# Kernel tuning notes

Hardware: AMD Instinct MI355X
Metric: run time of the kernel (lower is better)

## Reference

```python
import jax, jax.numpy as jnp
import numpy as np

HIDDEN = 128
B, N, S = 4, 200, 512  # batch, 200 segments, 512 tokens each (hard-coded in source view())


def setup_inputs() -> dict:
    key = jax.random.key(0)
    ks = jax.random.split(key, 7)
    query = jax.random.normal(ks[0], (B, HIDDEN), dtype=jnp.float32)
    context = jax.random.normal(ks[1], (B, N, S, HIDDEN), dtype=jnp.float32)
    context_mask = jax.random.uniform(ks[2], (B, N, S), dtype=jnp.float32)
    scale = 1.0 / np.sqrt(HIDDEN)
    Wq = jax.random.normal(ks[3], (HIDDEN, HIDDEN), dtype=jnp.float32) * scale
    bq = jax.random.normal(ks[4], (HIDDEN,), dtype=jnp.float32) * 0.01
    Wc = jax.random.normal(ks[5], (HIDDEN, HIDDEN), dtype=jnp.float32) * scale
    bc = jax.random.normal(ks[6], (HIDDEN,), dtype=jnp.float32) * 0.01
    return {"query": query, "context": context, "context_mask": context_mask,
            "Wq": Wq, "bq": bq, "Wc": Wc, "bc": bc}


def reference(query, context, context_mask, Wq, bq, Wc, bc):
    # q_projection / c_projection (nn.Linear: x @ W.T + b)
    q = query @ Wq.T + bq                      # [B, H]
    c = context @ Wc.T + bc                    # [B, N, S, H]
    # bmm(reshape_c, q) -> scores [B, N, S]
    att = jnp.einsum('bnsh,bh->bns', c, q)
    masked_att = att * context_mask            # multiplicative mask (as in source)
    w = jax.nn.softmax(masked_att, axis=-1)    # [B, N, S]
    # fused dual-axis weighted reductions (avoid [B,N,S,H] broadcast materialization)
    result = jnp.einsum('bns,bnsh->bnh', w, context)       # sum over tokens S
    token_result = jnp.einsum('bns,bnsh->bsh', w, context)  # sum over segments N
    return (result, token_result)
```

## Files before the change

### kernel.cpp

```cpp
#include <hip/hip_runtime.h>
#include <hip/hip_bf16.h>
#include <math.h>

#define H    128
#define NB   4
#define NSEG 200
#define NS   512
#define GN   10
#define GS   64
#define NGRP (NSEG / GN)
#define NST  (NS / GS)

#define RES4 (NB * NSEG * H / 4)
#define TOK4 (NB * NS * H / 4)


__global__ __launch_bounds__(512)
void precompute_kernel(const float* __restrict__ query,
                       const float* __restrict__ Wq,
                       const float* __restrict__ bq,
                       const float* __restrict__ Wc,
                       const float* __restrict__ bc,
                       float* __restrict__ v_out,
                       float* __restrict__ c0_out) {
    __shared__ float WqS[H * (H + 1)];
    __shared__ float qsh[H];
    __shared__ float redv[512];

    const int tid = threadIdx.x;
    const int b   = blockIdx.x;

    for (int i = tid; i < H * H; i += 512)
        WqS[(i >> 7) * (H + 1) + (i & 127)] = Wq[i];
    __syncthreads();

    if (tid < H) {
        float q = bq[tid];
        const float* qr = query + b * H;
        const float* wr = WqS + tid * (H + 1);
        #pragma unroll 8
        for (int k = 0; k < H; ++k) q += qr[k] * wr[k];
        qsh[tid] = q;
    }
    __syncthreads();

    const int h = tid & 127, part = tid >> 7;
    float vp = 0.f;
    #pragma unroll 8
    for (int k = part * 32; k < part * 32 + 32; ++k)
        vp += qsh[k] * Wc[k * H + h];
    redv[tid] = vp;
    __syncthreads();
    if (tid < H)
        v_out[b * H + tid] = redv[tid] + redv[tid + 128] + redv[tid + 256] + redv[tid + 384];

    if (tid < H) redv[tid] = qsh[tid] * bc[tid];
    __syncthreads();
    for (int off = 64; off > 0; off >>= 1) {
        if (tid < off && tid < H / 2) redv[tid] += redv[tid + off];
        __syncthreads();
    }
    if (tid == 0) c0_out[b] = redv[0];
}

__global__ __launch_bounds__(512)
void scores_softmax_kernel(const float* __restrict__ context,
                           const float* __restrict__ mask,
                           const float* __restrict__ v,
                           const float* __restrict__ c0,
                           float* __restrict__ w_out) {
    __shared__ float sc[NS];
    __shared__ float psum[16];
    __shared__ float zinv_sh;

    const int tid = threadIdx.x;
    const int blk = blockIdx.x;
    const int b   = blk / NSEG;
    const float* cseg = context + (size_t)blk * NS * H;
    const float* mrow = mask + (size_t)blk * NS;

    const int   h4  = tid & 31;
    const int   rg  = tid >> 5;
    const float4 vq = ((const float4*)(v + b * H))[h4];
    const float c0b = c0[b];

    float zpart = 0.f;
    #pragma unroll 8
    for (int it = 0; it < NS / 16; ++it) {
        const int s = it * 16 + rg;
        const float4 cv = ((const float4*)(cseg + (size_t)s * H))[h4];
        float p = cv.x * vq.x + cv.y * vq.y + cv.z * vq.z + cv.w * vq.w;
        p += __shfl_xor(p, 16);
        p += __shfl_xor(p, 8);
        p += __shfl_xor(p, 4);
        p += __shfl_xor(p, 2);
        p += __shfl_xor(p, 1);
        if (h4 == 0) {
            const float e = __expf(fminf((p + c0b) * mrow[s], 80.f));
            sc[s] = e;
            zpart += e;
        }
    }
    if (h4 == 0) psum[rg] = zpart;
    __syncthreads();
    if (tid < 64) {
        float t = (tid < 16) ? psum[tid] : 0.f;
        t += __shfl_xor(t, 8);
        t += __shfl_xor(t, 4);
        t += __shfl_xor(t, 2);
        t += __shfl_xor(t, 1);
        if (tid == 0) zinv_sh = 1.f / t;
    }
    __syncthreads();
    w_out[(size_t)blk * NS + tid] = sc[tid] * zinv_sh;
}

__global__ __launch_bounds__(512)
void weighted_kernel(const float* __restrict__ context,
                     const float* __restrict__ w,
                     float* __restrict__ result_part,
                     float* __restrict__ token_part) {
    const int bid = blockIdx.x;
    const int st  = bid & (NST - 1);
    const int tmp = bid / NST;
    const int ng  = tmp % NGRP;
    const int b   = tmp / NGRP;
    const int n0  = ng * GN;
    const int s0  = st * GS;

    const int tid = threadIdx.x;
    const int h4  = tid & 31;
    const int rg  = tid >> 5;

    __shared__ float  wt[GN * GS];
    __shared__ float4 red4[5 * 16 * 32];

    for (int i = tid; i < GN * GS; i += 512) {
        const int nn = i >> 6, ss = i & (GS - 1);
        wt[i] = w[((size_t)(b * NSEG + n0 + nn)) * NS + s0 + ss];
    }
    __syncthreads();

    float4 racc[GN];
    float4 tacc[4];
    #pragma unroll
    for (int n = 0; n < GN; ++n) racc[n] = make_float4(0.f, 0.f, 0.f, 0.f);
    #pragma unroll
    for (int j = 0; j < 4; ++j) tacc[j] = make_float4(0.f, 0.f, 0.f, 0.f);

    #pragma unroll
    for (int n = 0; n < GN; ++n) {
        const float* base = context + ((size_t)(b * NSEG + n0 + n) * NS + s0) * (size_t)H;
        #pragma unroll
        for (int j = 0; j < 4; ++j) {
            const int s = j * 16 + rg;
            const float  wv = wt[n * GS + s];
            const float4 cv = ((const float4*)(base + (size_t)s * H))[h4];
            racc[n].x += wv * cv.x; racc[n].y += wv * cv.y;
            racc[n].z += wv * cv.z; racc[n].w += wv * cv.w;
            tacc[j].x += wv * cv.x; tacc[j].y += wv * cv.y;
            tacc[j].z += wv * cv.z; tacc[j].w += wv * cv.w;
        }
    }

    #pragma unroll
    for (int j = 0; j < 4; ++j) {
        const int s = j * 16 + rg;
        ((float4*)token_part)[(((size_t)ng * NB + b) * NS + s0 + s) * 32 + h4] = tacc[j];
    }

    for (int nb = 0; nb < GN; nb += 5) {
        #pragma unroll
        for (int j = 0; j < 5; ++j)
            red4[(j * 16 + rg) * 32 + h4] = racc[nb + j];
        __syncthreads();
        for (int off = 8; off > 0; off >>= 1) {
            if (rg < off) {
                #pragma unroll
                for (int j = 0; j < 5; ++j) {
                    float4 o = red4[(j * 16 + rg + off) * 32 + h4];
                    float4 mm = red4[(j * 16 + rg) * 32 + h4];
                    mm.x += o.x; mm.y += o.y; mm.z += o.z; mm.w += o.w;
                    red4[(j * 16 + rg) * 32 + h4] = mm;
                }
            }
            __syncthreads();
        }
        if (rg == 0) {
            #pragma unroll
            for (int j = 0; j < 5; ++j)
                ((float4*)result_part)[(((size_t)(b * NSEG + n0 + nb + j)) * NST + st) * 32 + h4]
                    = red4[(j * 16) * 32 + h4];
        }
        __syncthreads();
    }
}

__global__ void combine_kernel(const float* __restrict__ rpart,
                               const float* __restrict__ tpart,
                               float* __restrict__ result_out,
                               float* __restrict__ token_out) {
    const int i = blockIdx.x * blockDim.x + threadIdx.x;
    if (i < RES4) {
        const int row = i >> 5, h4 = i & 31;
        float4 acc = {0.f, 0.f, 0.f, 0.f};
        const float4* p = (const float4*)rpart;
        #pragma unroll
        for (int st = 0; st < NST; ++st) {
            float4 o = p[((size_t)row * NST + st) * 32 + h4];
            acc.x += o.x; acc.y += o.y; acc.z += o.z; acc.w += o.w;
        }
        ((float4*)result_out)[i] = acc;
    } else {
        const int j = i - RES4;
        float4 acc = {0.f, 0.f, 0.f, 0.f};
        const float4* p = (const float4*)tpart;
        #pragma unroll
        for (int g = 0; g < NGRP; ++g) {
            float4 o = p[(size_t)g * TOK4 + j];
            acc.x += o.x; acc.y += o.y; acc.z += o.z; acc.w += o.w;
        }
        ((float4*)token_out)[j] = acc;
    }
}

extern "C" void kernel_launch(void* const* d_in, const int* in_sizes, int n_in,
                              void* d_out, int out_size, void* d_ws, size_t ws_size,
                              hipStream_t stream) {
    const float* query   = (const float*)d_in[0];
    const float* context = (const float*)d_in[1];
    const float* mask    = (const float*)d_in[2];
    const float* Wq      = (const float*)d_in[3];
    const float* bq      = (const float*)d_in[4];
    const float* Wc      = (const float*)d_in[5];
    const float* bc      = (const float*)d_in[6];

    float* out = (float*)d_out;
    float* wsf = (float*)d_ws;

    float* v     = wsf;
    float* c0    = wsf + 512;
    float* w     = wsf + 1024;
    float* rpart = wsf + 1024 + NB * NSEG * NS;
    float* tpart = rpart + NB * NSEG * NST * H;

    float* result_out = out;
    float* token_out  = out + NB * NSEG * H;

    precompute_kernel<<<NB, 512, 0, stream>>>(query, Wq, bq, Wc, bc, v, c0);
    scores_softmax_kernel<<<NB * NSEG, 512, 0, stream>>>(context, mask, v, c0, w);
    weighted_kernel<<<NB * NGRP * NST, 512, 0, stream>>>(context, w, rpart, tpart);
    combine_kernel<<<(RES4 + TOK4) / 256, 256, 0, stream>>>(rpart, tpart, result_out, token_out);
}
```

Measured before the change: 353.7 us.

## Fuse query/context projection precompute into scores kernel and enlarge segment group

Removes the separate precompute launch: each scores/softmax block recomputes q, v = Wc^T q and the bias dot c0 from Wq/Wc, which stay cache-resident. This saves one launch and one dependency bubble, at the cost of redundant projection work in all 800 blocks. The segment group size GN also grows from 10 to 25. That reduces the number of token partial sums written and later combined, but it means fewer weighted-kernel blocks (256 instead of 640) and more accumulator registers per thread.

Result: slower. 411.4 us (+16.3%).

```diff
diff --git a/kernel.cpp b/kernel.cpp
--- a/kernel.cpp
+++ b/kernel.cpp
@@ -6,7 +6,7 @@
 #define NB   4
 #define NSEG 200
 #define NS   512
-#define GN   10
+#define GN   25
 #define GS   64
 #define NGRP (NSEG / GN)
 #define NST  (NS / GS)
@@ -16,59 +16,18 @@
 
 
 __global__ __launch_bounds__(512)
-void precompute_kernel(const float* __restrict__ query,
-                       const float* __restrict__ Wq,
-                       const float* __restrict__ bq,
-                       const float* __restrict__ Wc,
-                       const float* __restrict__ bc,
-                       float* __restrict__ v_out,
-                       float* __restrict__ c0_out) {
-    __shared__ float WqS[H * (H + 1)];
+void scores_softmax_kernel(const float* __restrict__ query,
+                           const float* __restrict__ context,
+                           const float* __restrict__ mask,
+                           const float* __restrict__ Wq,
+                           const float* __restrict__ bq,
+                           const float* __restrict__ Wc,
+                           const float* __restrict__ bc,
+                           float* __restrict__ w_out) {
+    __shared__ float red[512];
     __shared__ float qsh[H];
-    __shared__ float redv[512];
-
-    const int tid = threadIdx.x;
-    const int b   = blockIdx.x;
-
-    for (int i = tid; i < H * H; i += 512)
-        WqS[(i >> 7) * (H + 1) + (i & 127)] = Wq[i];
-    __syncthreads();
-
-    if (tid < H) {
-        float q = bq[tid];
-        const float* qr = query + b * H;
-        const float* wr = WqS + tid * (H + 1);
-        #pragma unroll 8
-        for (int k = 0; k < H; ++k) q += qr[k] * wr[k];
-        qsh[tid] = q;
-    }
-    __syncthreads();
-
-    const int h = tid & 127, part = tid >> 7;
-    float vp = 0.f;
-    #pragma unroll 8
-    for (int k = part * 32; k < part * 32 + 32; ++k)
-        vp += qsh[k] * Wc[k * H + h];
-    redv[tid] = vp;
-    __syncthreads();
-    if (tid < H)
-        v_out[b * H + tid] = redv[tid] + redv[tid + 128] + redv[tid + 256] + redv[tid + 384];
-
-    if (tid < H) redv[tid] = qsh[tid] * bc[tid];
-    __syncthreads();
-    for (int off = 64; off > 0; off >>= 1) {
-        if (tid < off && tid < H / 2) redv[tid] += redv[tid + off];
-        __syncthreads();
-    }
-    if (tid == 0) c0_out[b] = redv[0];
-}
-
-__global__ __launch_bounds__(512)
-void scores_softmax_kernel(const float* __restrict__ context,
-                           const float* __restrict__ mask,
-                           const float* __restrict__ v,
-                           const float* __restrict__ c0,
-                           float* __restrict__ w_out) {
+    __shared__ float vsh[H];
+    __shared__ float c0sh;
     __shared__ float sc[NS];
     __shared__ float psum[16];
     __shared__ float zinv_sh;
@@ -76,13 +35,48 @@
     const int tid = threadIdx.x;
     const int blk = blockIdx.x;
     const int b   = blk / NSEG;
+
+    const int hh = tid & 127, pp = tid >> 7;
+    {
+        const float4* wr = (const float4*)(Wq + hh * H + pp * 32);
+        const float4* q4 = (const float4*)(query + b * H + pp * 32);
+        float qa = 0.f;
+        #pragma unroll
+        for (int k = 0; k < 8; ++k) {
+            const float4 wv = wr[k], qv = q4[k];
+            qa += wv.x * qv.x + wv.y * qv.y + wv.z * qv.z + wv.w * qv.w;
+        }
+        red[tid] = qa;
+    }
+    __syncthreads();
+    if (tid < H) qsh[tid] = red[tid] + red[tid + 128] + red[tid + 256] + red[tid + 384] + bq[tid];
+    __syncthreads();
+    {
+        float vp = 0.f;
+        #pragma unroll 8
+        for (int k = pp * 32; k < pp * 32 + 32; ++k) vp += qsh[k] * Wc[k * H + hh];
+        red[tid] = vp;
+    }
+    __syncthreads();
+    if (tid < H) {
+        vsh[tid] = red[tid] + red[tid + 128] + red[tid + 256] + red[tid + 384];
+        red[tid] = qsh[tid] * bc[tid];
+    }
+    __syncthreads();
+    if (tid < 64) {
+        float t = red[tid] + red[tid + 64];
+        t += __shfl_xor(t, 32); t += __shfl_xor(t, 16); t += __shfl_xor(t, 8);
+        t += __shfl_xor(t, 4);  t += __shfl_xor(t, 2);  t += __shfl_xor(t, 1);
+        if (tid == 0) c0sh = t;
+    }
+    __syncthreads();
+
     const float* cseg = context + (size_t)blk * NS * H;
     const float* mrow = mask + (size_t)blk * NS;
-
     const int   h4  = tid & 31;
     const int   rg  = tid >> 5;
-    const float4 vq = ((const float4*)(v + b * H))[h4];
-    const float c0b = c0[b];
+    const float4 vq = ((const float4*)vsh)[h4];
+    const float c0b = c0sh;
 
     float zpart = 0.f;
     #pragma unroll 8
@@ -238,8 +232,6 @@
     float* out = (float*)d_out;
     float* wsf = (float*)d_ws;
 
-    float* v     = wsf;
-    float* c0    = wsf + 512;
     float* w     = wsf + 1024;
     float* rpart = wsf + 1024 + NB * NSEG * NS;
     float* tpart = rpart + NB * NSEG * NST * H;
@@ -247,8 +239,7 @@
     float* result_out = out;
     float* token_out  = out + NB * NSEG * H;
 
-    precompute_kernel<<<NB, 512, 0, stream>>>(query, Wq, bq, Wc, bc, v, c0);
-    scores_softmax_kernel<<<NB * NSEG, 512, 0, stream>>>(context, mask, v, c0, w);
+    scores_softmax_kernel<<<NB * NSEG, 512, 0, stream>>>(query, context, mask, Wq, bq, Wc, bc, w);
     weighted_kernel<<<NB * NGRP * NST, 512, 0, stream>>>(context, w, rpart, tpart);
     combine_kernel<<<(RES4 + TOK4) / 256, 256, 0, stream>>>(rpart, tpart, result_out, token_out);
 }
```
